# Performance work log

Hardware: AMD Instinct MI355X
Metric: run time of the kernel (lower is better)

## Reference

```python
import jax, jax.numpy as jnp
import numpy as np

DT = 0.01          # Euler step size
ALPHA = 1.0        # Grubb exponent (hardcoded in forward())
V0 = 0.02          # resting venous blood volume fraction
NOISE_AMP = 0.01   # amplitude of per-step noise injected into the neural drive
T = 1000           # integration length (hardcoded in forward())
B = 16384          # batch of independent simulations


def setup_inputs() -> dict:
    key = jax.random.key(0)
    noise = jax.random.normal(key, (T, B), dtype=jnp.float32)
    f32 = lambda v: jnp.asarray(v, dtype=jnp.float32)
    return {
        "noise": noise,
        "sigma": f32(0.9),
        "mu": f32(0.8),
        "lamb": f32(0.3),
        "beta": f32(0.9),
        "psi": f32(0.5),
        "phi": f32(2.0),
        "chi": f32(0.3),
    }


def reference(noise, sigma, mu, lamb, beta, psi, phi, chi):
    # Balloon-Windkessel BOLD model, explicit Euler, per-step noise.
    # States per simulation: s (vasodilatory signal), f (flow), v (volume), q (dHb).
    b = noise.shape[1]
    inv_alpha = 1.0 / ALPHA

    def step(carry, z):
        s, f, v, q = carry
        # oxygen extraction fraction E(f) = 1 - (1 - E0)^(1/f)
        E = 1.0 - (1.0 - beta) ** (1.0 / f)
        v_a = v ** inv_alpha  # outflow v^(1/alpha)
        s2 = s + DT * (NOISE_AMP * z - sigma * s - mu * (f - 1.0))
        f2 = f + DT * s
        v2 = v + DT * (f - v_a) / lamb
        q2 = q + DT * (f * E / beta - v_a * q / v) / lamb
        # BOLD readout at the new state
        y = V0 * (phi * (1.0 - q2) + psi * (1.0 - q2 / v2) + chi * (1.0 - v2))
        return (s2, f2, v2, q2), y

    init = (
        jnp.zeros((b,), noise.dtype),
        jnp.ones((b,), noise.dtype),
        jnp.ones((b,), noise.dtype),
        jnp.ones((b,), noise.dtype),
    )
    _, ys = jax.lax.scan(step, init, noise)  # ys: [T, B]
    return ys
```

## Files before the change

kernel.cpp:

```cpp
#include <hip/hip_runtime.h>


#define BATCH     16384
#define DT        0.01f
#define NOISE_AMP 0.01f
#define V0        0.02f
#define CHUNKS    40
#define CL        25
#define TPB       256

#if __has_builtin(__builtin_amdgcn_exp2f)
#define EXP2F(x) __builtin_amdgcn_exp2f(x)
#else
#define EXP2F(x) exp2f(x)
#endif

__device__ __forceinline__ float uf(float x) {
    return __uint_as_float(__builtin_amdgcn_readfirstlane(__float_as_uint(x)));
}

struct D22 { double a, b, c, d; };
__device__ __forceinline__ D22 dmul(D22 x, D22 y) {
    D22 r;
    r.a = x.a * y.a + x.b * y.c;  r.b = x.a * y.b + x.b * y.d;
    r.c = x.c * y.a + x.d * y.c;  r.d = x.c * y.b + x.d * y.d;
    return r;
}

__device__ __forceinline__ D22 a25_of(float sigma, float mu) {
    D22 A; A.a = 1.0 - 0.01 * (double)sigma; A.b = -0.01 * (double)mu;
           A.c = 0.01;                       A.d = 1.0;
    D22 A2 = dmul(A, A), A4 = dmul(A2, A2), A8 = dmul(A4, A4);
    D22 A16 = dmul(A8, A8);
    return dmul(dmul(A16, A8), A);
}

__global__ __launch_bounds__(TPB, 8) void k_aggsf(
    const float* __restrict__ noise,
    const float* __restrict__ p_sigma,
    const float* __restrict__ p_mu,
    float* __restrict__ wsS, float* __restrict__ wsF)
{
    const int sim = blockIdx.x * TPB + threadIdx.x;
    const int cc  = blockIdx.y;

    const float sigma = uf(p_sigma[0]);
    const float mu    = uf(p_mu[0]);
    const float as_   = 1.0f - DT * sigma;
    const float dtn   = DT * NOISE_AMP;
    const float dtm   = DT * mu;

    const float* zp = noise + cc * (CL * BATCH) + sim;
    float rs = 0.0f, rf = 0.0f;
#pragma unroll
    for (int j = 0; j < CL; ++j) {
        const float z = zp[j * BATCH];
        const float u = __builtin_fmaf(dtn, z, dtm);
        const float t = __builtin_fmaf(as_, rs, __builtin_fmaf(-dtm, rf, u));
        rf = __builtin_fmaf(DT, rs, rf);
        rs = t;
    }
    wsS[cc * BATCH + sim] = rs;
    wsF[cc * BATCH + sim] = rf;
}

__global__ __launch_bounds__(TPB, 8) void k_scansf(
    const float* __restrict__ p_sigma,
    const float* __restrict__ p_mu,
    float* __restrict__ wsS, float* __restrict__ wsF)
{
    const int sim = blockIdx.x * TPB + threadIdx.x;
    const D22 P = a25_of(uf(p_sigma[0]), uf(p_mu[0]));

    double s = 0.0, f = 1.0;
#pragma unroll 8
    for (int c = 0; c < CHUNKS; ++c) {
        const int idx = c * BATCH + sim;
        const float rs = wsS[idx], rf = wsF[idx];
        wsS[idx] = (float)s; wsF[idx] = (float)f;
        const double ns = P.a * s + P.b * f + (double)rs;
        f               = P.c * s + P.d * f + (double)rf;
        s = ns;
    }
}

__global__ __launch_bounds__(TPB, 8) void k_aggvq(
    const float* __restrict__ noise,
    const float* __restrict__ p_sigma,
    const float* __restrict__ p_mu,
    const float* __restrict__ p_lamb,
    const float* __restrict__ p_beta,
    const float* __restrict__ wsS, const float* __restrict__ wsF,
    float* __restrict__ wsV, float* __restrict__ wsQ)
{
    const int sim = blockIdx.x * TPB + threadIdx.x;
    const int cc  = blockIdx.y;

    const float sigma = uf(p_sigma[0]);
    const float mu    = uf(p_mu[0]);
    const float lamb  = uf(p_lamb[0]);
    const float beta  = uf(p_beta[0]);

    const float as_   = 1.0f - DT * sigma;
    const float dtn   = DT * NOISE_AMP;
    const float dtm   = DT * mu;
    const float dt_il = uf((float)(0.01 / (double)lamb));
    const float av    = 1.0f - dt_il;
    const float kq    = uf(dt_il / beta);
    const float lc    = uf(log2f(1.0f - beta));

    float s = wsS[cc * BATCH + sim];
    float f = wsF[cc * BATCH + sim];

    const float* zp = noise + cc * (CL * BATCH) + sim;
    float Rv = 0.0f, Rq = 0.0f;
#pragma unroll
    for (int j = 0; j < CL; ++j) {
        const float z    = zp[j * BATCH];
        const float invf = __builtin_amdgcn_rcpf(f);
        const float e2   = EXP2F(lc * invf);
        const float t1   = __builtin_fmaf(-f, e2, f);
        Rv = __builtin_fmaf(av, Rv, dt_il * f);
        Rq = __builtin_fmaf(av, Rq, kq * t1);
        const float s2 = __builtin_fmaf(as_, s,
                         __builtin_fmaf(dtn, z,
                         __builtin_fmaf(-dtm, f, dtm)));
        f = __builtin_fmaf(DT, s, f);
        s = s2;
    }
    wsV[cc * BATCH + sim] = Rv;
    wsQ[cc * BATCH + sim] = Rq;
}

__global__ __launch_bounds__(TPB, 8) void k_scanvq(
    const float* __restrict__ p_lamb,
    float* __restrict__ wsV, float* __restrict__ wsQ)
{
    const int sim = blockIdx.x * TPB + threadIdx.x;
    const double avd = 1.0 - 0.01 / (double)uf(p_lamb[0]);
    const double av2 = avd * avd, av4 = av2 * av2, av8 = av4 * av4;
    const double av16 = av8 * av8;
    const double ap = av16 * av8 * avd;

    double v = 1.0, q = 1.0;
#pragma unroll 8
    for (int c = 0; c < CHUNKS; ++c) {
        const int idx = c * BATCH + sim;
        const float Rv = wsV[idx], Rq = wsQ[idx];
        wsV[idx] = (float)v; wsQ[idx] = (float)q;
        v = ap * v + (double)Rv;
        q = ap * q + (double)Rq;
    }
}

__global__ __launch_bounds__(TPB, 8) void k_emit(
    const float* __restrict__ noise,
    const float* __restrict__ p_sigma,
    const float* __restrict__ p_mu,
    const float* __restrict__ p_lamb,
    const float* __restrict__ p_beta,
    const float* __restrict__ p_psi,
    const float* __restrict__ p_phi,
    const float* __restrict__ p_chi,
    const float* __restrict__ wsS, const float* __restrict__ wsF,
    const float* __restrict__ wsV, const float* __restrict__ wsQ,
    float* __restrict__ out)
{
    const int sim = blockIdx.x * TPB + threadIdx.x;
    const int cc  = blockIdx.y;

    const float sigma = uf(p_sigma[0]);
    const float mu    = uf(p_mu[0]);
    const float lamb  = uf(p_lamb[0]);
    const float beta  = uf(p_beta[0]);
    const float psi   = uf(p_psi[0]);
    const float phi   = uf(p_phi[0]);
    const float chi   = uf(p_chi[0]);

    const float as_   = 1.0f - DT * sigma;
    const float dtn   = DT * NOISE_AMP;
    const float dtm   = DT * mu;
    const float dt_il = uf((float)(0.01 / (double)lamb));
    const float av    = 1.0f - dt_il;
    const float kq    = uf(dt_il / beta);
    const float lc    = uf(log2f(1.0f - beta));
    const float c0 = V0 * (phi + psi + chi), c1 = V0 * phi, c2 = V0 * psi, c3 = V0 * chi;

    float s = wsS[cc * BATCH + sim];
    float f = wsF[cc * BATCH + sim];
    float v = wsV[cc * BATCH + sim];
    float q = wsQ[cc * BATCH + sim];

    const float* zp = noise + cc * (CL * BATCH) + sim;
    float*       op = out   + cc * (CL * BATCH) + sim;

#pragma unroll
    for (int j = 0; j < CL; ++j) {
        const float z    = zp[j * BATCH];
        const float invf = __builtin_amdgcn_rcpf(f);
        const float e2   = EXP2F(lc * invf);
        const float t1   = __builtin_fmaf(-f, e2, f);
        const float vn   = __builtin_fmaf(av, v, dt_il * f);
        const float qn   = __builtin_fmaf(av, q, kq * t1);
        const float s2 = __builtin_fmaf(as_, s,
                         __builtin_fmaf(dtn, z,
                         __builtin_fmaf(-dtm, f, dtm)));
        f = __builtin_fmaf(DT, s, f);
        s = s2;

        const float invv = __builtin_amdgcn_rcpf(vn);
        const float y = __builtin_fmaf(-c2, qn * invv,
                        __builtin_fmaf(-c3, vn,
                        __builtin_fmaf(-c1, qn, c0)));
        __builtin_nontemporal_store(y, op + j * BATCH);
        v = vn; q = qn;
    }
}

#define CH0   20
#define CL0   50
#define GS0   32
#define NT0   (CH0 * GS0)

__global__ __launch_bounds__(NT0, 5) void balloon_mono(
    const float* __restrict__ noise,
    const float* __restrict__ p_sigma,
    const float* __restrict__ p_mu,
    const float* __restrict__ p_lamb,
    const float* __restrict__ p_beta,
    const float* __restrict__ p_psi,
    const float* __restrict__ p_phi,
    const float* __restrict__ p_chi,
    float* __restrict__ out)
{
    const int tid = threadIdx.x;
    const int g   = tid & (GS0 - 1);
    const int cc  = tid >> 5;
    const int sim = blockIdx.x * GS0 + g;

    const float sigma = uf(p_sigma[0]);
    const float mu    = uf(p_mu[0]);
    const float lamb  = uf(p_lamb[0]);
    const float beta  = uf(p_beta[0]);
    const float psi   = uf(p_psi[0]);
    const float phi   = uf(p_phi[0]);
    const float chi   = uf(p_chi[0]);

    const float as_   = 1.0f - DT * sigma;
    const float dtn   = DT * NOISE_AMP;
    const float dtm   = DT * mu;
    const float dt_il = uf((float)(0.01 / (double)lamb));
    const float av    = 1.0f - dt_il;
    const float kq    = uf(dt_il / beta);
    const float lc    = uf(log2f(1.0f - beta));
    const float c0 = V0 * (phi + psi + chi), c1 = V0 * phi, c2 = V0 * psi, c3 = V0 * chi;

    D22 A; A.a = 1.0 - 0.01 * (double)sigma; A.b = -0.01 * (double)mu;
           A.c = 0.01;                       A.d = 1.0;
    D22 A2 = dmul(A, A), A4 = dmul(A2, A2), A8 = dmul(A4, A4);
    D22 A16 = dmul(A8, A8), A32 = dmul(A16, A16);
    D22 P = dmul(dmul(A32, A16), A2);
    double avd = 1.0 - 0.01 / (double)lamb;
    double av2 = avd * avd, av4 = av2 * av2, av8 = av4 * av4;
    double av16 = av8 * av8, av32 = av16 * av16;
    double ap = av32 * av16 * av2;

    float M11[5], M12[5], M21[5], M22[5], AVP[5];
#pragma unroll
    for (int j = 0; j < 5; ++j) {
        M11[j] = uf((float)P.a); M12[j] = uf((float)P.b);
        M21[j] = uf((float)P.c); M22[j] = uf((float)P.d);
        AVP[j] = uf((float)ap);
        P = dmul(P, P); ap = ap * ap;
    }

    float ws_h = 0.0f, wf_h = 1.0f, avc = 1.0f;
#pragma unroll
    for (int j = 0; j < 5; ++j) {
        if ((cc >> j) & 1) {
            float t = __builtin_fmaf(M11[j], ws_h, M12[j] * wf_h);
            wf_h = __builtin_fmaf(M21[j], ws_h, M22[j] * wf_h);
            ws_h = t;
            avc *= AVP[j];
        }
    }

    __shared__ float sA[NT0];
    __shared__ float sB[NT0];

    const float* zp = noise + cc * (CL0 * BATCH) + sim;

    float rs = 0.0f, rf = 0.0f;
#pragma unroll 10
    for (int j = 0; j < CL0; ++j) {
        const float z = zp[j * BATCH];
        const float u = __builtin_fmaf(dtn, z, dtm);
        const float t = __builtin_fmaf(as_, rs, __builtin_fmaf(-dtm, rf, u));
        rf = __builtin_fmaf(DT, rs, rf);
        rs = t;
    }

    sA[tid] = rs; sB[tid] = rf;
    __syncthreads();
#pragma unroll
    for (int j = 0; j < 5; ++j) {
        const int off = 1 << j;
        float ns = 0.0f, nf = 0.0f;
        const bool has = (cc >= off);
        if (has) { ns = sA[tid - off * GS0]; nf = sB[tid - off * GS0]; }
        __syncthreads();
        if (has) {
            rs = __builtin_fmaf(M11[j], ns, __builtin_fmaf(M12[j], nf, rs));
            rf = __builtin_fmaf(M21[j], ns, __builtin_fmaf(M22[j], nf, rf));
            sA[tid] = rs; sB[tid] = rf;
        }
        __syncthreads();
    }
    float s0 = ws_h, f0 = wf_h;
    if (cc > 0) { s0 += sA[tid - GS0]; f0 += sB[tid - GS0]; }
    __syncthreads();

    float s = s0, f = f0, Rv = 0.0f, Rq = 0.0f;
#pragma unroll 10
    for (int j = 0; j < CL0; ++j) {
        const float z    = zp[j * BATCH];
        const float invf = __builtin_amdgcn_rcpf(f);
        const float e2   = EXP2F(lc * invf);
        const float t1   = __builtin_fmaf(-f, e2, f);
        Rv = __builtin_fmaf(av, Rv, dt_il * f);
        Rq = __builtin_fmaf(av, Rq, kq * t1);
        const float s2 = __builtin_fmaf(as_, s,
                         __builtin_fmaf(dtn, z,
                         __builtin_fmaf(-dtm, f, dtm)));
        f = __builtin_fmaf(DT, s, f);
        s = s2;
    }

    sA[tid] = Rv; sB[tid] = Rq;
    __syncthreads();
#pragma unroll
    for (int j = 0; j < 5; ++j) {
        const int off = 1 << j;
        float nv = 0.0f, nq = 0.0f;
        const bool has = (cc >= off);
        if (has) { nv = sA[tid - off * GS0]; nq = sB[tid - off * GS0]; }
        __syncthreads();
        if (has) {
            Rv = __builtin_fmaf(AVP[j], nv, Rv);
            Rq = __builtin_fmaf(AVP[j], nq, Rq);
            sA[tid] = Rv; sB[tid] = Rq;
        }
        __syncthreads();
    }
    float v = avc, q = avc;
    if (cc > 0) { v += sA[tid - GS0]; q += sB[tid - GS0]; }

    s = s0; f = f0;
    float* op = out + cc * (CL0 * BATCH) + sim;
#pragma unroll 10
    for (int j = 0; j < CL0; ++j) {
        const float z    = zp[j * BATCH];
        const float invf = __builtin_amdgcn_rcpf(f);
        const float e2   = EXP2F(lc * invf);
        const float t1   = __builtin_fmaf(-f, e2, f);
        const float vn   = __builtin_fmaf(av, v, dt_il * f);
        const float qn   = __builtin_fmaf(av, q, kq * t1);
        const float s2 = __builtin_fmaf(as_, s,
                         __builtin_fmaf(dtn, z,
                         __builtin_fmaf(-dtm, f, dtm)));
        f = __builtin_fmaf(DT, s, f);
        s = s2;

        const float invv = __builtin_amdgcn_rcpf(vn);
        const float y = __builtin_fmaf(-c2, qn * invv,
                        __builtin_fmaf(-c3, vn,
                        __builtin_fmaf(-c1, qn, c0)));
        op[j * BATCH] = y;
        v = vn; q = qn;
    }
}

extern "C" void kernel_launch(void* const* d_in, const int* in_sizes, int n_in,
                              void* d_out, int out_size, void* d_ws, size_t ws_size,
                              hipStream_t stream) {
    const float* noise   = (const float*)d_in[0];
    const float* p_sigma = (const float*)d_in[1];
    const float* p_mu    = (const float*)d_in[2];
    const float* p_lamb  = (const float*)d_in[3];
    const float* p_beta  = (const float*)d_in[4];
    const float* p_psi   = (const float*)d_in[5];
    const float* p_phi   = (const float*)d_in[6];
    const float* p_chi   = (const float*)d_in[7];

    const size_t narr = (size_t)CHUNKS * BATCH;
    const size_t need = 4 * narr * sizeof(float);
    if (d_ws != nullptr && ws_size >= need) {
        float* wsS = (float*)d_ws;
        float* wsF = wsS + narr;
        float* wsV = wsF + narr;
        float* wsQ = wsV + narr;

        const dim3 gStream(BATCH / TPB, CHUNKS);
        const int  gScan = BATCH / TPB;

        k_aggsf<<<gStream, TPB, 0, stream>>>(noise, p_sigma, p_mu, wsS, wsF);
        k_scansf<<<gScan, TPB, 0, stream>>>(p_sigma, p_mu, wsS, wsF);
        k_aggvq<<<gStream, TPB, 0, stream>>>(noise, p_sigma, p_mu, p_lamb, p_beta,
                                             wsS, wsF, wsV, wsQ);
        k_scanvq<<<gScan, TPB, 0, stream>>>(p_lamb, wsV, wsQ);
        k_emit<<<gStream, TPB, 0, stream>>>(noise, p_sigma, p_mu, p_lamb, p_beta,
                                            p_psi, p_phi, p_chi,
                                            wsS, wsF, wsV, wsQ, (float*)d_out);
    } else {
        balloon_mono<<<BATCH / GS0, NT0, 0, stream>>>(
            noise, p_sigma, p_mu, p_lamb, p_beta, p_psi, p_phi, p_chi,
            (float*)d_out);
    }
}
```

Baseline: 151.0 us.

## Replace s/f scan, v/q aggregation and scan, and emit with one sequential walk kernel

The five-kernel chunked-scan pipeline becomes two kernels. The s/f chunk aggregation stays; a new walk kernel runs each simulation sequentially through all 1000 steps. It carries the s/f chunk boundaries in double precision using the precomputed affine aggregates, and it carries v/q directly instead of building a parallel prefix for them. This removes three launches and the v/q workspace traffic, and noise for the next chunk is double-buffered in registers to hide load latency. The cost is far less parallelism: only 16384 threads in 256 blocks of 64, each running a long serial dependency chain, so occupancy and latency hiding on the GPU may be poor.

```diff
diff --git a/kernel.cpp b/kernel.cpp
--- a/kernel.cpp
+++ b/kernel.cpp
@@ -8,6 +8,7 @@
 #define CHUNKS    40
 #define CL        25
 #define TPB       256
+#define WTPB      64
 
 #if __has_builtin(__builtin_amdgcn_exp2f)
 #define EXP2F(x) __builtin_amdgcn_exp2f(x)
@@ -64,96 +65,7 @@
     wsF[cc * BATCH + sim] = rf;
 }
 
-__global__ __launch_bounds__(TPB, 8) void k_scansf(
-    const float* __restrict__ p_sigma,
-    const float* __restrict__ p_mu,
-    float* __restrict__ wsS, float* __restrict__ wsF)
-{
-    const int sim = blockIdx.x * TPB + threadIdx.x;
-    const D22 P = a25_of(uf(p_sigma[0]), uf(p_mu[0]));
-
-    double s = 0.0, f = 1.0;
-#pragma unroll 8
-    for (int c = 0; c < CHUNKS; ++c) {
-        const int idx = c * BATCH + sim;
-        const float rs = wsS[idx], rf = wsF[idx];
-        wsS[idx] = (float)s; wsF[idx] = (float)f;
-        const double ns = P.a * s + P.b * f + (double)rs;
-        f               = P.c * s + P.d * f + (double)rf;
-        s = ns;
-    }
-}
-
-__global__ __launch_bounds__(TPB, 8) void k_aggvq(
-    const float* __restrict__ noise,
-    const float* __restrict__ p_sigma,
-    const float* __restrict__ p_mu,
-    const float* __restrict__ p_lamb,
-    const float* __restrict__ p_beta,
-    const float* __restrict__ wsS, const float* __restrict__ wsF,
-    float* __restrict__ wsV, float* __restrict__ wsQ)
-{
-    const int sim = blockIdx.x * TPB + threadIdx.x;
-    const int cc  = blockIdx.y;
-
-    const float sigma = uf(p_sigma[0]);
-    const float mu    = uf(p_mu[0]);
-    const float lamb  = uf(p_lamb[0]);
-    const float beta  = uf(p_beta[0]);
-
-    const float as_   = 1.0f - DT * sigma;
-    const float dtn   = DT * NOISE_AMP;
-    const float dtm   = DT * mu;
-    const float dt_il = uf((float)(0.01 / (double)lamb));
-    const float av    = 1.0f - dt_il;
-    const float kq    = uf(dt_il / beta);
-    const float lc    = uf(log2f(1.0f - beta));
-
-    float s = wsS[cc * BATCH + sim];
-    float f = wsF[cc * BATCH + sim];
-
-    const float* zp = noise + cc * (CL * BATCH) + sim;
-    float Rv = 0.0f, Rq = 0.0f;
-#pragma unroll
-    for (int j = 0; j < CL; ++j) {
-        const float z    = zp[j * BATCH];
-        const float invf = __builtin_amdgcn_rcpf(f);
-        const float e2   = EXP2F(lc * invf);
-        const float t1   = __builtin_fmaf(-f, e2, f);
-        Rv = __builtin_fmaf(av, Rv, dt_il * f);
-        Rq = __builtin_fmaf(av, Rq, kq * t1);
-        const float s2 = __builtin_fmaf(as_, s,
-                         __builtin_fmaf(dtn, z,
-                         __builtin_fmaf(-dtm, f, dtm)));
-        f = __builtin_fmaf(DT, s, f);
-        s = s2;
-    }
-    wsV[cc * BATCH + sim] = Rv;
-    wsQ[cc * BATCH + sim] = Rq;
-}
-
-__global__ __launch_bounds__(TPB, 8) void k_scanvq(
-    const float* __restrict__ p_lamb,
-    float* __restrict__ wsV, float* __restrict__ wsQ)
-{
-    const int sim = blockIdx.x * TPB + threadIdx.x;
-    const double avd = 1.0 - 0.01 / (double)uf(p_lamb[0]);
-    const double av2 = avd * avd, av4 = av2 * av2, av8 = av4 * av4;
-    const double av16 = av8 * av8;
-    const double ap = av16 * av8 * avd;
-
-    double v = 1.0, q = 1.0;
-#pragma unroll 8
-    for (int c = 0; c < CHUNKS; ++c) {
-        const int idx = c * BATCH + sim;
-        const float Rv = wsV[idx], Rq = wsQ[idx];
-        wsV[idx] = (float)v; wsQ[idx] = (float)q;
-        v = ap * v + (double)Rv;
-        q = ap * q + (double)Rq;
-    }
-}
-
-__global__ __launch_bounds__(TPB, 8) void k_emit(
+__global__ __launch_bounds__(WTPB) void k_walk(
     const float* __restrict__ noise,
     const float* __restrict__ p_sigma,
     const float* __restrict__ p_mu,
@@ -163,11 +75,15 @@
     const float* __restrict__ p_phi,
     const float* __restrict__ p_chi,
     const float* __restrict__ wsS, const float* __restrict__ wsF,
-    const float* __restrict__ wsV, const float* __restrict__ wsQ,
     float* __restrict__ out)
 {
-    const int sim = blockIdx.x * TPB + threadIdx.x;
-    const int cc  = blockIdx.y;
+    const int sim = blockIdx.x * WTPB + threadIdx.x;
+    const float* zcol = noise + sim;
+    float*       ocol = out   + sim;
+
+    float zA[CL], zB[CL];
+#pragma unroll
+    for (int j = 0; j < CL; ++j) zA[j] = zcol[j * BATCH];
 
     const float sigma = uf(p_sigma[0]);
     const float mu    = uf(p_mu[0]);
@@ -186,35 +102,70 @@
     const float lc    = uf(log2f(1.0f - beta));
     const float c0 = V0 * (phi + psi + chi), c1 = V0 * phi, c2 = V0 * psi, c3 = V0 * chi;
 
-    float s = wsS[cc * BATCH + sim];
-    float f = wsF[cc * BATCH + sim];
-    float v = wsV[cc * BATCH + sim];
-    float q = wsQ[cc * BATCH + sim];
-
-    const float* zp = noise + cc * (CL * BATCH) + sim;
-    float*       op = out   + cc * (CL * BATCH) + sim;
-
-#pragma unroll
-    for (int j = 0; j < CL; ++j) {
-        const float z    = zp[j * BATCH];
-        const float invf = __builtin_amdgcn_rcpf(f);
-        const float e2   = EXP2F(lc * invf);
-        const float t1   = __builtin_fmaf(-f, e2, f);
-        const float vn   = __builtin_fmaf(av, v, dt_il * f);
-        const float qn   = __builtin_fmaf(av, q, kq * t1);
-        const float s2 = __builtin_fmaf(as_, s,
-                         __builtin_fmaf(dtn, z,
-                         __builtin_fmaf(-dtm, f, dtm)));
-        f = __builtin_fmaf(DT, s, f);
-        s = s2;
-
-        const float invv = __builtin_amdgcn_rcpf(vn);
-        const float y = __builtin_fmaf(-c2, qn * invv,
-                        __builtin_fmaf(-c3, vn,
-                        __builtin_fmaf(-c1, qn, c0)));
-        __builtin_nontemporal_store(y, op + j * BATCH);
-        v = vn; q = qn;
-    }
+    const D22 P = a25_of(sigma, mu);
+
+    double sd = 0.0, fd = 1.0;
+    float  v  = 1.0f, q = 1.0f;
+
+#define WALK_CHUNK(ZR, CBASE)                                               \
+    {                                                                       \
+        float s = (float)sd, f = (float)fd;                                 \
+        float* op = ocol + (size_t)(CBASE) * CL * BATCH;                    \
+        _Pragma("unroll")                                                   \
+        for (int j = 0; j < CL; ++j) {                                      \
+            const float z    = ZR[j];                                       \
+            const float invf = __builtin_amdgcn_rcpf(f);                    \
+            const float e2   = EXP2F(lc * invf);                            \
+            const float t1   = __builtin_fmaf(-f, e2, f);                   \
+            const float vn   = __builtin_fmaf(av, v, dt_il * f);            \
+            const float qn   = __builtin_fmaf(av, q, kq * t1);              \
+            const float s2   = __builtin_fmaf(as_, s,                       \
+                               __builtin_fmaf(dtn, z,                       \
+                               __builtin_fmaf(-dtm, f, dtm)));              \
+            f = __builtin_fmaf(DT, s, f);                                   \
+            s = s2;                                                         \
+            const float invv = __builtin_amdgcn_rcpf(vn);                   \
+            const float y = __builtin_fmaf(-c2, qn * invv,                  \
+                            __builtin_fmaf(-c3, vn,                         \
+                            __builtin_fmaf(-c1, qn, c0)));                  \
+            __builtin_nontemporal_store(y, op + j * BATCH);                 \
+            v = vn; q = qn;                                                 \
+        }                                                                   \
+    }
+
+    for (int c = 0; c < CHUNKS; c += 2) {
+        const float rsA = wsS[c * BATCH + sim];
+        const float rfA = wsF[c * BATCH + sim];
+        const float rsB = wsS[(c + 1) * BATCH + sim];
+        const float rfB = wsF[(c + 1) * BATCH + sim];
+
+        {
+            const float* zp = zcol + (size_t)(c + 1) * CL * BATCH;
+#pragma unroll
+            for (int j = 0; j < CL; ++j) zB[j] = zp[j * BATCH];
+        }
+
+        WALK_CHUNK(zA, c);
+        {
+            const double ns = P.a * sd + P.b * fd + (double)rsA;
+            fd              = P.c * sd + P.d * fd + (double)rfA;
+            sd = ns;
+        }
+
+        if (c + 2 < CHUNKS) {
+            const float* zp = zcol + (size_t)(c + 2) * CL * BATCH;
+#pragma unroll
+            for (int j = 0; j < CL; ++j) zA[j] = zp[j * BATCH];
+        }
+
+        WALK_CHUNK(zB, c + 1);
+        {
+            const double ns = P.a * sd + P.b * fd + (double)rsB;
+            fd              = P.c * sd + P.d * fd + (double)rfB;
+            sd = ns;
+        }
+    }
+#undef WALK_CHUNK
 }
 
 #define CH0   20
@@ -393,24 +344,16 @@
     const float* p_chi   = (const float*)d_in[7];
 
     const size_t narr = (size_t)CHUNKS * BATCH;
-    const size_t need = 4 * narr * sizeof(float);
+    const size_t need = 2 * narr * sizeof(float);
     if (d_ws != nullptr && ws_size >= need) {
         float* wsS = (float*)d_ws;
         float* wsF = wsS + narr;
-        float* wsV = wsF + narr;
-        float* wsQ = wsV + narr;
-
-        const dim3 gStream(BATCH / TPB, CHUNKS);
-        const int  gScan = BATCH / TPB;
-
-        k_aggsf<<<gStream, TPB, 0, stream>>>(noise, p_sigma, p_mu, wsS, wsF);
-        k_scansf<<<gScan, TPB, 0, stream>>>(p_sigma, p_mu, wsS, wsF);
-        k_aggvq<<<gStream, TPB, 0, stream>>>(noise, p_sigma, p_mu, p_lamb, p_beta,
-                                             wsS, wsF, wsV, wsQ);
-        k_scanvq<<<gScan, TPB, 0, stream>>>(p_lamb, wsV, wsQ);
-        k_emit<<<gStream, TPB, 0, stream>>>(noise, p_sigma, p_mu, p_lamb, p_beta,
-                                            p_psi, p_phi, p_chi,
-                                            wsS, wsF, wsV, wsQ, (float*)d_out);
+
+        k_aggsf<<<dim3(BATCH / TPB, CHUNKS), TPB, 0, stream>>>(
+            noise, p_sigma, p_mu, wsS, wsF);
+        k_walk<<<BATCH / WTPB, WTPB, 0, stream>>>(
+            noise, p_sigma, p_mu, p_lamb, p_beta, p_psi, p_phi, p_chi,
+            wsS, wsF, (float*)d_out);
     } else {
         balloon_mono<<<BATCH / GS0, NT0, 0, stream>>>(
             noise, p_sigma, p_mu, p_lamb, p_beta, p_psi, p_phi, p_chi,
```

New measurement: 171.1 us. 1.13x slower.

## Fold chunk-carry scans into consumer kernels and use fewer longer chunks

Applied to the files above, without the earlier changes.

Removes the two separate scan kernels. Each block of the vq and emit kernels now recomputes its chunk's starting state by walking the earlier chunks' aggregates in double precision, and the chunk count drops from 40 to 8 with 125 steps per chunk. This cuts the launch count from five to three and removes the workspace read-modify-write passes. In exchange, the grid has far fewer blocks (64x8), which reduces parallelism and latency hiding, and the redundant prefix work is unevenly spread across chunks.

```diff
diff --git a/kernel.cpp b/kernel.cpp
--- a/kernel.cpp
+++ b/kernel.cpp
@@ -5,8 +5,8 @@
 #define DT        0.01f
 #define NOISE_AMP 0.01f
 #define V0        0.02f
-#define CHUNKS    40
-#define CL        25
+#define CHUNKS    8
+#define CL        125
 #define TPB       256
 
 #if __has_builtin(__builtin_amdgcn_exp2f)
@@ -27,19 +27,26 @@
     return r;
 }
 
-__device__ __forceinline__ D22 a25_of(float sigma, float mu) {
+__device__ __forceinline__ D22 a125_of(float sigma, float mu) {
     D22 A; A.a = 1.0 - 0.01 * (double)sigma; A.b = -0.01 * (double)mu;
            A.c = 0.01;                       A.d = 1.0;
     D22 A2 = dmul(A, A), A4 = dmul(A2, A2), A8 = dmul(A4, A4);
-    D22 A16 = dmul(A8, A8);
-    return dmul(dmul(A16, A8), A);
-}
-
-__global__ __launch_bounds__(TPB, 8) void k_aggsf(
+    D22 A16 = dmul(A8, A8), A32 = dmul(A16, A16), A64 = dmul(A32, A32);
+    return dmul(dmul(dmul(dmul(dmul(A64, A32), A16), A8), A4), A);
+}
+
+__device__ __forceinline__ double av125_of(float lamb) {
+    const double avd = 1.0 - 0.01 / (double)lamb;
+    const double av2 = avd * avd, av4 = av2 * av2, av8 = av4 * av4;
+    const double av16 = av8 * av8, av32 = av16 * av16, av64 = av32 * av32;
+    return av64 * av32 * av16 * av8 * av4 * avd;
+}
+
+__global__ __launch_bounds__(TPB, 4) void k_aggsf(
     const float* __restrict__ noise,
     const float* __restrict__ p_sigma,
     const float* __restrict__ p_mu,
-    float* __restrict__ wsS, float* __restrict__ wsF)
+    float* __restrict__ wsRS, float* __restrict__ wsRF)
 {
     const int sim = blockIdx.x * TPB + threadIdx.x;
     const int cc  = blockIdx.y;
@@ -50,48 +57,28 @@
     const float dtn   = DT * NOISE_AMP;
     const float dtm   = DT * mu;
 
-    const float* zp = noise + cc * (CL * BATCH) + sim;
+    const float* zp = noise + (size_t)cc * (CL * BATCH) + sim;
     float rs = 0.0f, rf = 0.0f;
-#pragma unroll
+#pragma unroll 25
     for (int j = 0; j < CL; ++j) {
-        const float z = zp[j * BATCH];
+        const float z = zp[(size_t)j * BATCH];
         const float u = __builtin_fmaf(dtn, z, dtm);
         const float t = __builtin_fmaf(as_, rs, __builtin_fmaf(-dtm, rf, u));
         rf = __builtin_fmaf(DT, rs, rf);
         rs = t;
     }
-    wsS[cc * BATCH + sim] = rs;
-    wsF[cc * BATCH + sim] = rf;
-}
-
-__global__ __launch_bounds__(TPB, 8) void k_scansf(
-    const float* __restrict__ p_sigma,
-    const float* __restrict__ p_mu,
-    float* __restrict__ wsS, float* __restrict__ wsF)
-{
-    const int sim = blockIdx.x * TPB + threadIdx.x;
-    const D22 P = a25_of(uf(p_sigma[0]), uf(p_mu[0]));
-
-    double s = 0.0, f = 1.0;
-#pragma unroll 8
-    for (int c = 0; c < CHUNKS; ++c) {
-        const int idx = c * BATCH + sim;
-        const float rs = wsS[idx], rf = wsF[idx];
-        wsS[idx] = (float)s; wsF[idx] = (float)f;
-        const double ns = P.a * s + P.b * f + (double)rs;
-        f               = P.c * s + P.d * f + (double)rf;
-        s = ns;
-    }
-}
-
-__global__ __launch_bounds__(TPB, 8) void k_aggvq(
+    wsRS[cc * BATCH + sim] = rs;
+    wsRF[cc * BATCH + sim] = rf;
+}
+
+__global__ __launch_bounds__(TPB, 4) void k_vq(
     const float* __restrict__ noise,
     const float* __restrict__ p_sigma,
     const float* __restrict__ p_mu,
     const float* __restrict__ p_lamb,
     const float* __restrict__ p_beta,
-    const float* __restrict__ wsS, const float* __restrict__ wsF,
-    float* __restrict__ wsV, float* __restrict__ wsQ)
+    const float* __restrict__ wsRS, const float* __restrict__ wsRF,
+    float* __restrict__ wsRV, float* __restrict__ wsRQ)
 {
     const int sim = blockIdx.x * TPB + threadIdx.x;
     const int cc  = blockIdx.y;
@@ -109,14 +96,22 @@
     const float kq    = uf(dt_il / beta);
     const float lc    = uf(log2f(1.0f - beta));
 
-    float s = wsS[cc * BATCH + sim];
-    float f = wsF[cc * BATCH + sim];
-
-    const float* zp = noise + cc * (CL * BATCH) + sim;
+    const D22 P = a125_of(sigma, mu);
+    double sd = 0.0, fd = 1.0;
+    for (int k = 0; k < cc; ++k) {
+        const double rs = (double)wsRS[k * BATCH + sim];
+        const double rf = (double)wsRF[k * BATCH + sim];
+        const double ns = P.a * sd + P.b * fd + rs;
+        fd              = P.c * sd + P.d * fd + rf;
+        sd = ns;
+    }
+    float s = (float)sd, f = (float)fd;
+
+    const float* zp = noise + (size_t)cc * (CL * BATCH) + sim;
     float Rv = 0.0f, Rq = 0.0f;
-#pragma unroll
+#pragma unroll 25
     for (int j = 0; j < CL; ++j) {
-        const float z    = zp[j * BATCH];
+        const float z    = zp[(size_t)j * BATCH];
         const float invf = __builtin_amdgcn_rcpf(f);
         const float e2   = EXP2F(lc * invf);
         const float t1   = __builtin_fmaf(-f, e2, f);
@@ -128,32 +123,11 @@
         f = __builtin_fmaf(DT, s, f);
         s = s2;
     }
-    wsV[cc * BATCH + sim] = Rv;
-    wsQ[cc * BATCH + sim] = Rq;
-}
-
-__global__ __launch_bounds__(TPB, 8) void k_scanvq(
-    const float* __restrict__ p_lamb,
-    float* __restrict__ wsV, float* __restrict__ wsQ)
-{
-    const int sim = blockIdx.x * TPB + threadIdx.x;
-    const double avd = 1.0 - 0.01 / (double)uf(p_lamb[0]);
-    const double av2 = avd * avd, av4 = av2 * av2, av8 = av4 * av4;
-    const double av16 = av8 * av8;
-    const double ap = av16 * av8 * avd;
-
-    double v = 1.0, q = 1.0;
-#pragma unroll 8
-    for (int c = 0; c < CHUNKS; ++c) {
-        const int idx = c * BATCH + sim;
-        const float Rv = wsV[idx], Rq = wsQ[idx];
-        wsV[idx] = (float)v; wsQ[idx] = (float)q;
-        v = ap * v + (double)Rv;
-        q = ap * q + (double)Rq;
-    }
-}
-
-__global__ __launch_bounds__(TPB, 8) void k_emit(
+    wsRV[cc * BATCH + sim] = Rv;
+    wsRQ[cc * BATCH + sim] = Rq;
+}
+
+__global__ __launch_bounds__(TPB, 4) void k_emit(
     const float* __restrict__ noise,
     const float* __restrict__ p_sigma,
     const float* __restrict__ p_mu,
@@ -162,8 +136,8 @@
     const float* __restrict__ p_psi,
     const float* __restrict__ p_phi,
     const float* __restrict__ p_chi,
-    const float* __restrict__ wsS, const float* __restrict__ wsF,
-    const float* __restrict__ wsV, const float* __restrict__ wsQ,
+    const float* __restrict__ wsRS, const float* __restrict__ wsRF,
+    const float* __restrict__ wsRV, const float* __restrict__ wsRQ,
     float* __restrict__ out)
 {
     const int sim = blockIdx.x * TPB + threadIdx.x;
@@ -186,17 +160,31 @@
     const float lc    = uf(log2f(1.0f - beta));
     const float c0 = V0 * (phi + psi + chi), c1 = V0 * phi, c2 = V0 * psi, c3 = V0 * chi;
 
-    float s = wsS[cc * BATCH + sim];
-    float f = wsF[cc * BATCH + sim];
-    float v = wsV[cc * BATCH + sim];
-    float q = wsQ[cc * BATCH + sim];
-
-    const float* zp = noise + cc * (CL * BATCH) + sim;
-    float*       op = out   + cc * (CL * BATCH) + sim;
-
-#pragma unroll
+    const D22 P = a125_of(sigma, mu);
+    double sd = 0.0, fd = 1.0;
+    for (int k = 0; k < cc; ++k) {
+        const double rs = (double)wsRS[k * BATCH + sim];
+        const double rf = (double)wsRF[k * BATCH + sim];
+        const double ns = P.a * sd + P.b * fd + rs;
+        fd              = P.c * sd + P.d * fd + rf;
+        sd = ns;
+    }
+    float s = (float)sd, f = (float)fd;
+
+    const double ap = av125_of(lamb);
+    double vd = 1.0, qd = 1.0;
+    for (int k = 0; k < cc; ++k) {
+        vd = ap * vd + (double)wsRV[k * BATCH + sim];
+        qd = ap * qd + (double)wsRQ[k * BATCH + sim];
+    }
+    float v = (float)vd, q = (float)qd;
+
+    const float* zp = noise + (size_t)cc * (CL * BATCH) + sim;
+    float*       op = out   + (size_t)cc * (CL * BATCH) + sim;
+
+#pragma unroll 25
     for (int j = 0; j < CL; ++j) {
-        const float z    = zp[j * BATCH];
+        const float z    = zp[(size_t)j * BATCH];
         const float invf = __builtin_amdgcn_rcpf(f);
         const float e2   = EXP2F(lc * invf);
         const float t1   = __builtin_fmaf(-f, e2, f);
@@ -212,7 +200,7 @@
         const float y = __builtin_fmaf(-c2, qn * invv,
                         __builtin_fmaf(-c3, vn,
                         __builtin_fmaf(-c1, qn, c0)));
-        __builtin_nontemporal_store(y, op + j * BATCH);
+        __builtin_nontemporal_store(y, op + (size_t)j * BATCH);
         v = vn; q = qn;
     }
 }
@@ -395,22 +383,18 @@
     const size_t narr = (size_t)CHUNKS * BATCH;
     const size_t need = 4 * narr * sizeof(float);
     if (d_ws != nullptr && ws_size >= need) {
-        float* wsS = (float*)d_ws;
-        float* wsF = wsS + narr;
-        float* wsV = wsF + narr;
-        float* wsQ = wsV + narr;
-
-        const dim3 gStream(BATCH / TPB, CHUNKS);
-        const int  gScan = BATCH / TPB;
-
-        k_aggsf<<<gStream, TPB, 0, stream>>>(noise, p_sigma, p_mu, wsS, wsF);
-        k_scansf<<<gScan, TPB, 0, stream>>>(p_sigma, p_mu, wsS, wsF);
-        k_aggvq<<<gStream, TPB, 0, stream>>>(noise, p_sigma, p_mu, p_lamb, p_beta,
-                                             wsS, wsF, wsV, wsQ);
-        k_scanvq<<<gScan, TPB, 0, stream>>>(p_lamb, wsV, wsQ);
-        k_emit<<<gStream, TPB, 0, stream>>>(noise, p_sigma, p_mu, p_lamb, p_beta,
-                                            p_psi, p_phi, p_chi,
-                                            wsS, wsF, wsV, wsQ, (float*)d_out);
+        float* wsRS = (float*)d_ws;
+        float* wsRF = wsRS + narr;
+        float* wsRV = wsRF + narr;
+        float* wsRQ = wsRV + narr;
+
+        const dim3 g(BATCH / TPB, CHUNKS);
+        k_aggsf<<<g, TPB, 0, stream>>>(noise, p_sigma, p_mu, wsRS, wsRF);
+        k_vq<<<g, TPB, 0, stream>>>(noise, p_sigma, p_mu, p_lamb, p_beta,
+                                    wsRS, wsRF, wsRV, wsRQ);
+        k_emit<<<g, TPB, 0, stream>>>(noise, p_sigma, p_mu, p_lamb, p_beta,
+                                      p_psi, p_phi, p_chi,
+                                      wsRS, wsRF, wsRV, wsRQ, (float*)d_out);
     } else {
         balloon_mono<<<BATCH / GS0, NT0, 0, stream>>>(
             noise, p_sigma, p_mu, p_lamb, p_beta, p_psi, p_phi, p_chi,
```

New measurement: 173.8 us. +15.1%, slower.
